# Optimization experiments

Hardware: AMD Instinct MI355X
Metric: run time of the kernel (lower is better)

## Reference

```python
import jax, jax.numpy as jnp
import numpy as np

N = 20000      # nodes
E = 640000     # edges
IN = 2         # in_dim
H = 4          # heads
C = 64         # hidden_dim (per-head channels)
ED = 3         # edge_dim
K = 4          # num_clusters
EPS = 1e-16    # PyG softmax eps


def setup_inputs():
    key = jax.random.key(0)
    ks = jax.random.split(key, 32)
    g = lambda i, sh: (jax.random.normal(ks[i], sh, dtype=jnp.float32) * 0.1)
    inp = {
        'x': jax.random.normal(ks[0], (N, IN), dtype=jnp.float32),
        'edge_index': jax.random.randint(ks[1], (2, E), 0, N, dtype=jnp.int64),
        'edge_attr': jax.random.normal(ks[2], (E, ED), dtype=jnp.float32),
        # input_proj
        'Wp': g(3, (IN, C)), 'bp': g(4, (C,)),
        # conv1: in C -> H*C, concat
        'W1': g(5, (C, H * C)), 'We1': g(6, (ED, H * C)),
        'as1': g(7, (H, C)), 'ad1': g(8, (H, C)), 'ae1': g(9, (H, C)), 'b1': g(10, (H * C,)),
        # conv2: in H*C -> H*C, concat
        'W2': g(11, (H * C, H * C)), 'We2': g(12, (ED, H * C)),
        'as2': g(13, (H, C)), 'ad2': g(14, (H, C)), 'ae2': g(15, (H, C)), 'b2': g(16, (H * C,)),
        # conv3: in H*C -> C, heads=1
        'W3': g(17, (H * C, C)), 'We3': g(18, (ED, C)),
        'as3': g(19, (1, C)), 'ad3': g(20, (1, C)), 'ae3': g(21, (1, C)), 'b3': g(22, (C,)),
        # classifier
        'Wc': g(23, (C, K)), 'bc': g(24, (K,)),
    }
    return inp


def _gat(h, src, dst, edge_attr, W, We, a_src, a_dst, a_edge, bias, heads, cph):
    """PyG GATConv (shared lin for src/dst, edge_dim, concat=True), eval mode."""
    xh = (h @ W).reshape(N, heads, cph)                       # [N,H,C]
    alpha_src = jnp.einsum('nhc,hc->nh', xh, a_src)           # [N,H]
    alpha_dst = jnp.einsum('nhc,hc->nh', xh, a_dst)
    eh = (edge_attr @ We).reshape(E, heads, cph)              # [E,H,C]
    alpha = alpha_src[src] + alpha_dst[dst] + jnp.einsum('ehc,hc->eh', eh, a_edge)
    alpha = jax.nn.leaky_relu(alpha, 0.2)                     # [E,H]
    # segment softmax over destination neighborhoods
    m = jax.ops.segment_max(alpha, dst, num_segments=N)       # [N,H]
    ea = jnp.exp(alpha - m[dst])
    s = jax.ops.segment_sum(ea, dst, num_segments=N)
    attn = ea / (s[dst] + EPS)                                # [E,H]
    msg = xh[src] * attn[:, :, None]                          # [E,H,C]
    out = jax.ops.segment_sum(msg, dst, num_segments=N)       # [N,H,C]
    return out.reshape(N, heads * cph) + bias


def reference(x, edge_index, edge_attr, Wp, bp,
              W1, We1, as1, ad1, ae1, b1,
              W2, We2, as2, ad2, ae2, b2,
              W3, We3, as3, ad3, ae3, b3,
              Wc, bc):
    src, dst = edge_index[0], edge_index[1]
    h = jax.nn.elu(x @ Wp + bp)
    h = jax.nn.elu(_gat(h, src, dst, edge_attr, W1, We1, as1, ad1, ae1, b1, H, C))
    h = jax.nn.elu(_gat(h, src, dst, edge_attr, W2, We2, as2, ad2, ae2, b2, H, C))
    h = _gat(h, src, dst, edge_attr, W3, We3, as3, ad3, ae3, b3, 1, C)
    return jax.nn.softmax(h @ Wc + bc, axis=-1)
```

## Files before the change

### kernel.cpp

```cpp
#include <hip/hip_runtime.h>
#include <math.h>

#define N_NODES 20000
#define N_EDGES 640000

typedef __attribute__((ext_vector_type(8))) short short8;
typedef __attribute__((ext_vector_type(4))) float floatx4;
typedef __attribute__((ext_vector_type(2))) float float2v;

__device__ __forceinline__ float elu_f(float v) { return v > 0.f ? v : expm1f(v); }

__device__ __forceinline__ unsigned short bf16_rne(float f) {
  union { float f; unsigned u; } v;
  v.f = f;
  unsigned r = v.u + 0x7FFF + ((v.u >> 16) & 1);
  return (unsigned short)(r >> 16);
}

__device__ __forceinline__ float bf_to_f(unsigned short u) {
  union { unsigned u; float f; } v;
  v.u = (unsigned)u << 16;
  return v.f;
}

__device__ __forceinline__ float2v unpack_bf2(unsigned u) {
  union { unsigned u; float f; } lo, hi;
  lo.u = u << 16;
  hi.u = u & 0xffff0000u;
  return (float2v){lo.f, hi.f};
}

__device__ __forceinline__ int swz(int c) {
  return (c & ~7) | ((((c & 7) + ((c >> 3) >> 2))) & 7);
}


__global__ void zero_int_kernel(int* p, int n) {
  int i = blockIdx.x * 256 + threadIdx.x;
  if (i < n) p[i] = 0;
}

__global__ void hist_kernel(const int* __restrict__ dst, int* __restrict__ cnt, int ne) {
  int e = blockIdx.x * 256 + threadIdx.x;
  if (e < ne) atomicAdd(&cnt[dst[e]], 1);
}

__global__ __launch_bounds__(1024) void scan_kernel(const int* __restrict__ cnt,
                                                    int* __restrict__ row_ptr,
                                                    int* __restrict__ row_next, int n) {
  __shared__ int part[1024];
  int t = threadIdx.x;
  int per = (n + 1023) / 1024;
  int base = t * per;
  int local = 0;
  for (int i = 0; i < per; ++i) {
    int idx = base + i;
    if (idx < n) local += cnt[idx];
  }
  part[t] = local;
  __syncthreads();
  for (int off = 1; off < 1024; off <<= 1) {
    int v = (t >= off) ? part[t - off] : 0;
    __syncthreads();
    part[t] += v;
    __syncthreads();
  }
  int prefix = (t == 0) ? 0 : part[t - 1];
  for (int i = 0; i < per; ++i) {
    int idx = base + i;
    if (idx < n) {
      row_ptr[idx] = prefix;
      row_next[idx] = prefix;
      prefix += cnt[idx];
    }
  }
  if (t == 1023) row_ptr[n] = part[1023];
}

__global__ void fill_kernel(const int* __restrict__ dst, int* __restrict__ row_next,
                            int* __restrict__ csr_eid, int ne) {
  int e = blockIdx.x * 256 + threadIdx.x;
  if (e >= ne) return;
  int pos = atomicAdd(&row_next[dst[e]], 1);
  csr_eid[pos] = e;
}


__global__ void prep_all_kernel(const float* __restrict__ x, const float* __restrict__ Wp,
                                const float* __restrict__ bp, unsigned short* __restrict__ h_bf,
                                const float* __restrict__ W1, const float* __restrict__ W2,
                                const float* __restrict__ W3, unsigned short* __restrict__ Bt1,
                                unsigned short* __restrict__ Bt2, unsigned short* __restrict__ Bt3,
                                const float* __restrict__ We1, const float* __restrict__ ae1,
                                const float* __restrict__ We2, const float* __restrict__ ae2,
                                const float* __restrict__ We3, const float* __restrict__ ae3,
                                float* __restrict__ proj) {
  int b = blockIdx.x, t = threadIdx.x;
  if (b < 5000) {
    int i = b * 256 + t;
    int node = i >> 6, c = i & 63;
    float v = x[node * 2] * Wp[c] + x[node * 2 + 1] * Wp[64 + c] + bp[c];
    h_bf[i] = bf16_rne(elu_f(v));
  } else if (b < 5384) {
    int idx = (b - 5000) * 256 + t;
    const float* W; unsigned short* Bt; int K, Nc, local;
    if (idx < 16384)      { W = W1; Bt = Bt1; K = 64;  Nc = 256; local = idx; }
    else if (idx < 81920) { W = W2; Bt = Bt2; K = 256; Nc = 256; local = idx - 16384; }
    else if (idx < 98304) { W = W3; Bt = Bt3; K = 256; Nc = 64;  local = idx - 81920; }
    else return;
    int k = local / Nc, n = local - k * Nc;
    Bt[(size_t)n * K + k] = bf16_rne(W[local]);
  } else {
    if (t < 12) {
      int d = t >> 2, h = t & 3;
      float s = 0.f;
      for (int c = 0; c < 64; ++c) s += We1[d * 256 + h * 64 + c] * ae1[h * 64 + c];
      proj[t] = s;
    } else if (t < 24) {
      int u = t - 12; int d = u >> 2, h = u & 3;
      float s = 0.f;
      for (int c = 0; c < 64; ++c) s += We2[d * 256 + h * 64 + c] * ae2[h * 64 + c];
      proj[12 + u] = s;
    } else if (t < 27) {
      int d = t - 24;
      float s = 0.f;
      for (int c = 0; c < 64; ++c) s += We3[d * 64 + c] * ae3[c];
      proj[24 + d] = s;
    }
  }
}


__global__ void edge_prep_kernel(const int* __restrict__ csr_eid, const int* __restrict__ src,
                                 const float* __restrict__ ea, const float* __restrict__ proj,
                                 int* __restrict__ csr_src, float* __restrict__ edot) {
  int i = blockIdx.x * 256 + threadIdx.x;
  if (i >= N_EDGES) return;
  int eid = csr_eid[i];
  csr_src[i] = src[eid];
  float e0 = ea[eid * 3 + 0], e1 = ea[eid * 3 + 1], e2 = ea[eid * 3 + 2];
  #pragma unroll
  for (int h = 0; h < 4; ++h)
    edot[(size_t)h * N_EDGES + i] = e0 * proj[h] + e1 * proj[4 + h] + e2 * proj[8 + h];
  #pragma unroll
  for (int h = 0; h < 4; ++h)
    edot[(size_t)(4 + h) * N_EDGES + i] = e0 * proj[12 + h] + e1 * proj[16 + h] + e2 * proj[20 + h];
  edot[(size_t)8 * N_EDGES + i] = e0 * proj[24] + e1 * proj[25] + e2 * proj[26];
}


template <int KDIM>
__global__ __launch_bounds__(256) void mfma_gemm_alpha_kernel(
    const unsigned short* __restrict__ A, const unsigned short* __restrict__ Bt,
    unsigned short* __restrict__ C_bf, const float* __restrict__ a_src,
    const float* __restrict__ a_dst, float* __restrict__ alp_s,
    float* __restrict__ alp_d, int M, int Nc) {
  __shared__ unsigned short As[64][40];
  __shared__ unsigned short Bs[64][40];
  int t = threadIdx.x;
  int wave = t >> 6, lane = t & 63;
  int m_frag = lane & 15, quad = lane >> 4;
  int row0 = blockIdx.y * 64, col0 = blockIdx.x * 64;
  int lr = t >> 2;
  int lk = (t & 3) * 8;
  floatx4 acc[4];
  #pragma unroll
  for (int c = 0; c < 4; ++c) acc[c] = (floatx4){0.f, 0.f, 0.f, 0.f};

  for (int k0 = 0; k0 < KDIM; k0 += 32) {
    int gr = row0 + lr;
    short8 av = {0, 0, 0, 0, 0, 0, 0, 0};
    if (gr < M) av = *(const short8*)(A + (size_t)gr * KDIM + k0 + lk);
    *(short8*)(&As[lr][lk]) = av;
    short8 bv = *(const short8*)(Bt + (size_t)(col0 + lr) * KDIM + k0 + lk);
    *(short8*)(&Bs[lr][lk]) = bv;
    __syncthreads();
    short8 a = *(const short8*)(&As[wave * 16 + m_frag][quad * 8]);
    #pragma unroll
    for (int c = 0; c < 4; ++c) {
      short8 b = *(const short8*)(&Bs[c * 16 + m_frag][quad * 8]);
      acc[c] = __builtin_amdgcn_mfma_f32_16x16x32_bf16(a, b, acc[c], 0, 0, 0);
    }
    __syncthreads();
  }

  int H = Nc >> 6;
  int head = blockIdx.x;
  float ps[4] = {}, pd[4] = {};
  #pragma unroll
  for (int c = 0; c < 4; ++c) {
    float asv = a_src[head * 64 + c * 16 + m_frag];
    float adv = a_dst[head * 64 + c * 16 + m_frag];
    #pragma unroll
    for (int i = 0; i < 4; ++i) {
      ps[i] += acc[c][i] * asv;
      pd[i] += acc[c][i] * adv;
    }
  }
  #pragma unroll
  for (int off = 1; off < 16; off <<= 1) {
    #pragma unroll
    for (int i = 0; i < 4; ++i) {
      ps[i] += __shfl_xor(ps[i], off);
      pd[i] += __shfl_xor(pd[i], off);
    }
  }
  #pragma unroll
  for (int c = 0; c < 4; ++c) {
    #pragma unroll
    for (int i = 0; i < 4; ++i) {
      int gr = row0 + wave * 16 + quad * 4 + i;
      if (gr < M) C_bf[(size_t)gr * Nc + col0 + c * 16 + m_frag] = bf16_rne(acc[c][i]);
    }
  }
  if (m_frag == 0) {
    #pragma unroll
    for (int i = 0; i < 4; ++i) {
      int gr = row0 + wave * 16 + quad * 4 + i;
      if (gr < M) {
        alp_s[gr * H + head] = ps[i];
        alp_d[gr * H + head] = pd[i];
      }
    }
  }
}


template <bool OUT_BF>
__global__ __launch_bounds__(256) void softagg4_kernel(
    const int* __restrict__ row_ptr, const int* __restrict__ csr_src,
    const float* __restrict__ edot, const float* __restrict__ alp_s,
    const float* __restrict__ alp_d, const unsigned short* __restrict__ xh_bf,
    const float* __restrict__ bias, float* __restrict__ out,
    unsigned short* __restrict__ out_bf) {
  constexpr int HC = 256, H = 4, CHUNK = 256, L = 32, S = 8;
  __shared__ float lds_w[H][CHUNK + 8];
  __shared__ int lds_src[CHUNK];
  __shared__ float sh_r[H];
  __shared__ float sh_inv[H];
  __shared__ float red[4 * HC];

  int n = blockIdx.x;
  int t = threadIdx.x;
  int wave = t >> 6, lane = t & 63;
  int slot = t / L, l = t % L;
  int head2 = (8 * l) >> 6;
  int s0 = row_ptr[n], s1 = row_ptr[n + 1];

  float m_run = -INFINITY, s_run = 0.f;
  float2v accp[4] = {};
  float adv = alp_d[n * H + wave];
  const float* __restrict__ edot_h = edot + (size_t)wave * N_EDGES;

  for (int c0 = s0; c0 < s1; c0 += CHUNK) {
    int cend = min(s1, c0 + CHUNK);
    {
      int h = wave;
      float cm = -INFINITY;
      for (int i = c0 + lane; i < cend; i += 64) {
        int s = csr_src[i];
        if (h == 0) lds_src[i - c0] = s;
        float a = alp_s[s * H + h] + adv + edot_h[i];
        a = a > 0.f ? a : 0.2f * a;
        lds_w[h][i - c0] = a;
        cm = fmaxf(cm, a);
      }
      #pragma unroll
      for (int off = 1; off < 64; off <<= 1) cm = fmaxf(cm, __shfl_xor(cm, off));
      float m_new = fmaxf(m_run, cm);
      float r = __expf(m_run - m_new);
      float se = 0.f;
      for (int i = c0 + lane; i < cend; i += 64) {
        float w = __expf(lds_w[h][i - c0] - m_new);
        lds_w[h][i - c0] = w;
        se += w;
      }
      #pragma unroll
      for (int off = 1; off < 64; off <<= 1) se += __shfl_xor(se, off);
      s_run = s_run * r + se;
      m_run = m_new;
      if (lane == 0) sh_r[h] = r;
    }
    __syncthreads();
    float2v rrp = {sh_r[head2], sh_r[head2]};
    #pragma unroll
    for (int d = 0; d < 4; ++d) accp[d] *= rrp;
    int i = c0 + slot;
    for (; i + S < cend; i += 2 * S) {
      int sA = lds_src[i - c0];
      int sB = lds_src[i - c0 + S];
      float wA = lds_w[head2][i - c0];
      float wB = lds_w[head2][i - c0 + S];
      uint4 uA = *(const uint4*)(xh_bf + (size_t)sA * HC + l * 8);
      uint4 uB = *(const uint4*)(xh_bf + (size_t)sB * HC + l * 8);
      float2v wAp = {wA, wA}, wBp = {wB, wB};
      accp[0] = __builtin_elementwise_fma(unpack_bf2(uA.x), wAp, accp[0]);
      accp[1] = __builtin_elementwise_fma(unpack_bf2(uA.y), wAp, accp[1]);
      accp[2] = __builtin_elementwise_fma(unpack_bf2(uA.z), wAp, accp[2]);
      accp[3] = __builtin_elementwise_fma(unpack_bf2(uA.w), wAp, accp[3]);
      accp[0] = __builtin_elementwise_fma(unpack_bf2(uB.x), wBp, accp[0]);
      accp[1] = __builtin_elementwise_fma(unpack_bf2(uB.y), wBp, accp[1]);
      accp[2] = __builtin_elementwise_fma(unpack_bf2(uB.z), wBp, accp[2]);
      accp[3] = __builtin_elementwise_fma(unpack_bf2(uB.w), wBp, accp[3]);
    }
    if (i < cend) {
      int s = lds_src[i - c0];
      float w = lds_w[head2][i - c0];
      uint4 u = *(const uint4*)(xh_bf + (size_t)s * HC + l * 8);
      float2v wp = {w, w};
      accp[0] = __builtin_elementwise_fma(unpack_bf2(u.x), wp, accp[0]);
      accp[1] = __builtin_elementwise_fma(unpack_bf2(u.y), wp, accp[1]);
      accp[2] = __builtin_elementwise_fma(unpack_bf2(u.z), wp, accp[2]);
      accp[3] = __builtin_elementwise_fma(unpack_bf2(u.w), wp, accp[3]);
    }
    __syncthreads();
  }
  if (lane == 0) sh_inv[wave] = 1.0f / (s_run + 1e-16f);
  __syncthreads();
  float2v invp = {sh_inv[head2], sh_inv[head2]};
  #pragma unroll
  for (int d = 0; d < 4; ++d) accp[d] *= invp;
  float accf[8];
  #pragma unroll
  for (int d = 0; d < 4; ++d) { accf[2 * d] = accp[d].x; accf[2 * d + 1] = accp[d].y; }
  #pragma unroll
  for (int off = L; off < 64; off <<= 1) {
    #pragma unroll
    for (int j = 0; j < 8; ++j) accf[j] += __shfl_xor(accf[j], off);
  }
  if (lane < L) {
    #pragma unroll
    for (int j = 0; j < 8; ++j) red[wave * HC + swz(lane * 8 + j)] = accf[j];
  }
  __syncthreads();
  {
    int pos = swz(t & (HC - 1));
    float a = red[0 * HC + pos] + red[1 * HC + pos] + red[2 * HC + pos] + red[3 * HC + pos];
    a += bias[t];
    a = elu_f(a);
    if (OUT_BF) out_bf[(size_t)n * HC + t] = bf16_rne(a);
    else out[(size_t)n * HC + t] = a;
  }
}


__global__ __launch_bounds__(256) void softagg_cls_kernel(
    const int* __restrict__ row_ptr, const int* __restrict__ csr_src,
    const float* __restrict__ edot, const float* __restrict__ alp_s,
    const float* __restrict__ alp_d, const unsigned short* __restrict__ xh_bf,
    const float* __restrict__ b3, const float* __restrict__ Wc,
    const float* __restrict__ bc, float* __restrict__ out, int n_nodes) {
  constexpr int CHUNK = 256;
  __shared__ float lds_w[4][CHUNK];
  __shared__ int lds_s[4][CHUNK];

  int wave = threadIdx.x >> 6, lane = threadIdx.x & 63;
  int n = blockIdx.x * 4 + wave;
  if (n >= n_nodes) return;
  int slot = lane >> 3, l = lane & 7;
  int s0 = row_ptr[n], s1 = row_ptr[n + 1];

  float m_run = -INFINITY, s_run = 0.f;
  float2v accp[4] = {};
  float adv = alp_d[n];

  for (int c0 = s0; c0 < s1; c0 += CHUNK) {
    int cend = min(s1, c0 + CHUNK);
    float cm = -INFINITY;
    for (int i = c0 + lane; i < cend; i += 64) {
      int s = csr_src[i];
      lds_s[wave][i - c0] = s;
      float a = alp_s[s] + adv + edot[i];
      a = a > 0.f ? a : 0.2f * a;
      lds_w[wave][i - c0] = a;
      cm = fmaxf(cm, a);
    }
    #pragma unroll
    for (int off = 1; off < 64; off <<= 1) cm = fmaxf(cm, __shfl_xor(cm, off));
    float m_new = fmaxf(m_run, cm);
    float r = __expf(m_run - m_new);
    float se = 0.f;
    for (int i = c0 + lane; i < cend; i += 64) {
      float w = __expf(lds_w[wave][i - c0] - m_new);
      lds_w[wave][i - c0] = w;
      se += w;
    }
    #pragma unroll
    for (int off = 1; off < 64; off <<= 1) se += __shfl_xor(se, off);
    s_run = s_run * r + se;
    m_run = m_new;
    float2v rp = {r, r};
    #pragma unroll
    for (int d = 0; d < 4; ++d) accp[d] *= rp;
    for (int i = c0 + slot; i < cend; i += 8) {
      int s = lds_s[wave][i - c0];
      float w = lds_w[wave][i - c0];
      uint4 u = *(const uint4*)(xh_bf + (size_t)s * 64 + l * 8);
      float2v wp = {w, w};
      accp[0] = __builtin_elementwise_fma(unpack_bf2(u.x), wp, accp[0]);
      accp[1] = __builtin_elementwise_fma(unpack_bf2(u.y), wp, accp[1]);
      accp[2] = __builtin_elementwise_fma(unpack_bf2(u.z), wp, accp[2]);
      accp[3] = __builtin_elementwise_fma(unpack_bf2(u.w), wp, accp[3]);
    }
  }
  float inv = 1.0f / (s_run + 1e-16f);
  float2v invp = {inv, inv};
  #pragma unroll
  for (int d = 0; d < 4; ++d) accp[d] *= invp;
  float accf[8];
  #pragma unroll
  for (int d = 0; d < 4; ++d) { accf[2 * d] = accp[d].x; accf[2 * d + 1] = accp[d].y; }
  #pragma unroll
  for (int off = 8; off < 64; off <<= 1) {
    #pragma unroll
    for (int j = 0; j < 8; ++j) accf[j] += __shfl_xor(accf[j], off);
  }
  float p0 = 0.f, p1 = 0.f, p2 = 0.f, p3 = 0.f;
  #pragma unroll
  for (int j = 0; j < 8; ++j) {
    int c = l * 8 + j;
    float v = accf[j] + b3[c];
    p0 += v * Wc[c * 4 + 0];
    p1 += v * Wc[c * 4 + 1];
    p2 += v * Wc[c * 4 + 2];
    p3 += v * Wc[c * 4 + 3];
  }
  #pragma unroll
  for (int off = 1; off < 8; off <<= 1) {
    p0 += __shfl_xor(p0, off);
    p1 += __shfl_xor(p1, off);
    p2 += __shfl_xor(p2, off);
    p3 += __shfl_xor(p3, off);
  }
  if (lane == 0) {
    p0 += bc[0]; p1 += bc[1]; p2 += bc[2]; p3 += bc[3];
    float mx = fmaxf(fmaxf(p0, p1), fmaxf(p2, p3));
    float e0 = __expf(p0 - mx), e1 = __expf(p1 - mx), e2 = __expf(p2 - mx), e3 = __expf(p3 - mx);
    float s = 1.f / (e0 + e1 + e2 + e3);
    out[n * 4 + 0] = e0 * s;
    out[n * 4 + 1] = e1 * s;
    out[n * 4 + 2] = e2 * s;
    out[n * 4 + 3] = e3 * s;
  }
}


extern "C" void kernel_launch(void* const* d_in, const int* in_sizes, int n_in,
                              void* d_out, int out_size, void* d_ws, size_t ws_size,
                              hipStream_t stream) {
  const float* x   = (const float*)d_in[0];
  const int*   ei  = (const int*)d_in[1];
  const float* ea  = (const float*)d_in[2];
  const float* Wp  = (const float*)d_in[3];
  const float* bp  = (const float*)d_in[4];
  const float* W1  = (const float*)d_in[5];
  const float* We1 = (const float*)d_in[6];
  const float* as1 = (const float*)d_in[7];
  const float* ad1 = (const float*)d_in[8];
  const float* ae1 = (const float*)d_in[9];
  const float* b1  = (const float*)d_in[10];
  const float* W2  = (const float*)d_in[11];
  const float* We2 = (const float*)d_in[12];
  const float* as2 = (const float*)d_in[13];
  const float* ad2 = (const float*)d_in[14];
  const float* ae2 = (const float*)d_in[15];
  const float* b2  = (const float*)d_in[16];
  const float* W3  = (const float*)d_in[17];
  const float* We3 = (const float*)d_in[18];
  const float* as3 = (const float*)d_in[19];
  const float* ad3 = (const float*)d_in[20];
  const float* ae3 = (const float*)d_in[21];
  const float* b3  = (const float*)d_in[22];
  const float* Wc  = (const float*)d_in[23];
  const float* bc  = (const float*)d_in[24];
  float* out = (float*)d_out;

  const int* src = ei;
  const int* dst = ei + N_EDGES;

  char* wptr = (char*)d_ws;
  auto alloc = [&](size_t bytes) {
    char* p = wptr;
    wptr += (bytes + 255) & ~(size_t)255;
    return p;
  };
  int*            cnt      = (int*)alloc((size_t)N_NODES * 4);
  int*            row_ptr  = (int*)alloc((size_t)(N_NODES + 1) * 4);
  int*            row_next = (int*)alloc((size_t)N_NODES * 4);
  int*            csr_eid  = (int*)alloc((size_t)N_EDGES * 4);
  int*            csr_src  = (int*)alloc((size_t)N_EDGES * 4);
  float*          edot     = (float*)alloc((size_t)9 * N_EDGES * 4);
  unsigned short* hA_bf    = (unsigned short*)alloc((size_t)N_NODES * 256 * 2);
  unsigned short* hX_bf    = (unsigned short*)alloc((size_t)N_NODES * 256 * 2);
  float*          alp_s    = (float*)alloc((size_t)N_NODES * 4 * 4);
  float*          alp_d    = (float*)alloc((size_t)N_NODES * 4 * 4);
  float*          proj     = (float*)alloc(32 * 4);
  unsigned short* Bt1      = (unsigned short*)alloc((size_t)64 * 256 * 2);
  unsigned short* Bt2      = (unsigned short*)alloc((size_t)256 * 256 * 2);
  unsigned short* Bt3      = (unsigned short*)alloc((size_t)256 * 64 * 2);

  zero_int_kernel<<<(N_NODES + 255) / 256, 256, 0, stream>>>(cnt, N_NODES);
  hist_kernel<<<(N_EDGES + 255) / 256, 256, 0, stream>>>(dst, cnt, N_EDGES);
  scan_kernel<<<1, 1024, 0, stream>>>(cnt, row_ptr, row_next, N_NODES);
  fill_kernel<<<(N_EDGES + 255) / 256, 256, 0, stream>>>(dst, row_next, csr_eid, N_EDGES);

  prep_all_kernel<<<5385, 256, 0, stream>>>(x, Wp, bp, hA_bf, W1, W2, W3, Bt1, Bt2, Bt3,
                                            We1, ae1, We2, ae2, We3, ae3, proj);
  edge_prep_kernel<<<(N_EDGES + 255) / 256, 256, 0, stream>>>(csr_eid, src, ea, proj,
                                                              csr_src, edot);

  dim3 g256(4, (N_NODES + 63) / 64);
  dim3 g64(1, (N_NODES + 63) / 64);

  mfma_gemm_alpha_kernel<64><<<g256, 256, 0, stream>>>(hA_bf, Bt1, hX_bf, as1, ad1,
                                                       alp_s, alp_d, N_NODES, 256);
  softagg4_kernel<true><<<N_NODES, 256, 0, stream>>>(row_ptr, csr_src,
                                                     edot + (size_t)0 * N_EDGES,
                                                     alp_s, alp_d, hX_bf, b1, nullptr, hA_bf);

  mfma_gemm_alpha_kernel<256><<<g256, 256, 0, stream>>>(hA_bf, Bt2, hX_bf, as2, ad2,
                                                        alp_s, alp_d, N_NODES, 256);
  softagg4_kernel<true><<<N_NODES, 256, 0, stream>>>(row_ptr, csr_src,
                                                     edot + (size_t)4 * N_EDGES,
                                                     alp_s, alp_d, hX_bf, b2, nullptr, hA_bf);

  mfma_gemm_alpha_kernel<256><<<g64, 256, 0, stream>>>(hA_bf, Bt3, hX_bf, as3, ad3,
                                                       alp_s, alp_d, N_NODES, 64);
  softagg_cls_kernel<<<(N_NODES + 3) / 4, 256, 0, stream>>>(row_ptr, csr_src,
                                                            edot + (size_t)8 * N_EDGES,
                                                            alp_s, alp_d, hX_bf, b3, Wc, bc,
                                                            out, N_NODES);
}
```

Measured before the change: 396.3 us.

## Fuse edge prep into prep kernel and widen per-lane gather in aggregation

Merges the edge-prep kernel into the prep kernel: each edge block recomputes the 27 edge projection scalars into shared memory rather than reading them from a separate global buffer, which removes one launch and a dependency. In the layer-1/2 aggregation kernel, each lane now gathers 16 bf16 channels (two 16-byte loads) with 16 edge slots instead of 8 channels with 8 slots. The final cross-wave reduction uses a padded 3D shared array in place of the swizzled buffer. The zeroing kernel is replaced by hipMemsetAsync. Recomputing the projections in every edge block adds redundant work, and the wider per-lane accumulators raise register pressure.

```diff
diff --git a/kernel.cpp b/kernel.cpp
--- a/kernel.cpp
+++ b/kernel.cpp
@@ -30,15 +30,6 @@
   return (float2v){lo.f, hi.f};
 }
 
-__device__ __forceinline__ int swz(int c) {
-  return (c & ~7) | ((((c & 7) + ((c >> 3) >> 2))) & 7);
-}
-
-
-__global__ void zero_int_kernel(int* p, int n) {
-  int i = blockIdx.x * 256 + threadIdx.x;
-  if (i < n) p[i] = 0;
-}
 
 __global__ void hist_kernel(const int* __restrict__ dst, int* __restrict__ cnt, int ne) {
   int e = blockIdx.x * 256 + threadIdx.x;
@@ -94,7 +85,9 @@
                                 const float* __restrict__ We1, const float* __restrict__ ae1,
                                 const float* __restrict__ We2, const float* __restrict__ ae2,
                                 const float* __restrict__ We3, const float* __restrict__ ae3,
-                                float* __restrict__ proj) {
+                                const int* __restrict__ csr_eid, const int* __restrict__ src,
+                                const float* __restrict__ ea, int* __restrict__ csr_src,
+                                float* __restrict__ edot) {
   int b = blockIdx.x, t = threadIdx.x;
   if (b < 5000) {
     int i = b * 256 + t;
@@ -111,41 +104,37 @@
     int k = local / Nc, n = local - k * Nc;
     Bt[(size_t)n * K + k] = bf16_rne(W[local]);
   } else {
+    __shared__ float pj[27];
     if (t < 12) {
       int d = t >> 2, h = t & 3;
       float s = 0.f;
       for (int c = 0; c < 64; ++c) s += We1[d * 256 + h * 64 + c] * ae1[h * 64 + c];
-      proj[t] = s;
+      pj[t] = s;
     } else if (t < 24) {
       int u = t - 12; int d = u >> 2, h = u & 3;
       float s = 0.f;
       for (int c = 0; c < 64; ++c) s += We2[d * 256 + h * 64 + c] * ae2[h * 64 + c];
-      proj[12 + u] = s;
+      pj[12 + u] = s;
     } else if (t < 27) {
       int d = t - 24;
       float s = 0.f;
       for (int c = 0; c < 64; ++c) s += We3[d * 64 + c] * ae3[c];
-      proj[24 + d] = s;
-    }
-  }
-}
-
-
-__global__ void edge_prep_kernel(const int* __restrict__ csr_eid, const int* __restrict__ src,
-                                 const float* __restrict__ ea, const float* __restrict__ proj,
-                                 int* __restrict__ csr_src, float* __restrict__ edot) {
-  int i = blockIdx.x * 256 + threadIdx.x;
-  if (i >= N_EDGES) return;
-  int eid = csr_eid[i];
-  csr_src[i] = src[eid];
-  float e0 = ea[eid * 3 + 0], e1 = ea[eid * 3 + 1], e2 = ea[eid * 3 + 2];
-  #pragma unroll
-  for (int h = 0; h < 4; ++h)
-    edot[(size_t)h * N_EDGES + i] = e0 * proj[h] + e1 * proj[4 + h] + e2 * proj[8 + h];
-  #pragma unroll
-  for (int h = 0; h < 4; ++h)
-    edot[(size_t)(4 + h) * N_EDGES + i] = e0 * proj[12 + h] + e1 * proj[16 + h] + e2 * proj[20 + h];
-  edot[(size_t)8 * N_EDGES + i] = e0 * proj[24] + e1 * proj[25] + e2 * proj[26];
+      pj[24 + d] = s;
+    }
+    __syncthreads();
+    int i = (b - 5384) * 256 + t;
+    if (i >= N_EDGES) return;
+    int eid = csr_eid[i];
+    csr_src[i] = src[eid];
+    float e0 = ea[eid * 3 + 0], e1 = ea[eid * 3 + 1], e2 = ea[eid * 3 + 2];
+    #pragma unroll
+    for (int h = 0; h < 4; ++h)
+      edot[(size_t)h * N_EDGES + i] = e0 * pj[h] + e1 * pj[4 + h] + e2 * pj[8 + h];
+    #pragma unroll
+    for (int h = 0; h < 4; ++h)
+      edot[(size_t)(4 + h) * N_EDGES + i] = e0 * pj[12 + h] + e1 * pj[16 + h] + e2 * pj[20 + h];
+    edot[(size_t)8 * N_EDGES + i] = e0 * pj[24] + e1 * pj[25] + e2 * pj[26];
+  }
 }
 
 
@@ -233,36 +222,35 @@
     const float* __restrict__ alp_d, const unsigned short* __restrict__ xh_bf,
     const float* __restrict__ bias, float* __restrict__ out,
     unsigned short* __restrict__ out_bf) {
-  constexpr int HC = 256, H = 4, CHUNK = 256, L = 32, S = 8;
+  constexpr int HC = 256, H = 4, CHUNK = 256, S = 16;
   __shared__ float lds_w[H][CHUNK + 8];
   __shared__ int lds_src[CHUNK];
   __shared__ float sh_r[H];
   __shared__ float sh_inv[H];
-  __shared__ float red[4 * HC];
+  __shared__ float red2[4][16][17];
 
   int n = blockIdx.x;
   int t = threadIdx.x;
   int wave = t >> 6, lane = t & 63;
-  int slot = t / L, l = t % L;
-  int head2 = (8 * l) >> 6;
+  int slot = t >> 4, l = t & 15;
+  int head2 = l >> 2;
   int s0 = row_ptr[n], s1 = row_ptr[n + 1];
 
   float m_run = -INFINITY, s_run = 0.f;
-  float2v accp[4] = {};
+  float2v accp[8] = {};
   float adv = alp_d[n * H + wave];
   const float* __restrict__ edot_h = edot + (size_t)wave * N_EDGES;
 
   for (int c0 = s0; c0 < s1; c0 += CHUNK) {
     int cend = min(s1, c0 + CHUNK);
     {
-      int h = wave;
       float cm = -INFINITY;
       for (int i = c0 + lane; i < cend; i += 64) {
         int s = csr_src[i];
-        if (h == 0) lds_src[i - c0] = s;
-        float a = alp_s[s * H + h] + adv + edot_h[i];
+        if (wave == 0) lds_src[i - c0] = s;
+        float a = alp_s[s * H + wave] + adv + edot_h[i];
         a = a > 0.f ? a : 0.2f * a;
-        lds_w[h][i - c0] = a;
+        lds_w[wave][i - c0] = a;
         cm = fmaxf(cm, a);
       }
       #pragma unroll
@@ -271,47 +259,65 @@
       float r = __expf(m_run - m_new);
       float se = 0.f;
       for (int i = c0 + lane; i < cend; i += 64) {
-        float w = __expf(lds_w[h][i - c0] - m_new);
-        lds_w[h][i - c0] = w;
+        float w = __expf(lds_w[wave][i - c0] - m_new);
+        lds_w[wave][i - c0] = w;
         se += w;
       }
       #pragma unroll
       for (int off = 1; off < 64; off <<= 1) se += __shfl_xor(se, off);
       s_run = s_run * r + se;
       m_run = m_new;
-      if (lane == 0) sh_r[h] = r;
+      if (lane == 0) sh_r[wave] = r;
     }
     __syncthreads();
     float2v rrp = {sh_r[head2], sh_r[head2]};
     #pragma unroll
-    for (int d = 0; d < 4; ++d) accp[d] *= rrp;
+    for (int d = 0; d < 8; ++d) accp[d] *= rrp;
     int i = c0 + slot;
     for (; i + S < cend; i += 2 * S) {
       int sA = lds_src[i - c0];
       int sB = lds_src[i - c0 + S];
       float wA = lds_w[head2][i - c0];
       float wB = lds_w[head2][i - c0 + S];
-      uint4 uA = *(const uint4*)(xh_bf + (size_t)sA * HC + l * 8);
-      uint4 uB = *(const uint4*)(xh_bf + (size_t)sB * HC + l * 8);
+      const uint4* pA = (const uint4*)(xh_bf + (size_t)sA * HC + l * 16);
+      const uint4* pB = (const uint4*)(xh_bf + (size_t)sB * HC + l * 16);
+      uint4 a0 = pA[0];
+      uint4 a1 = pA[1];
+      uint4 b0 = pB[0];
+      uint4 b1 = pB[1];
       float2v wAp = {wA, wA}, wBp = {wB, wB};
-      accp[0] = __builtin_elementwise_fma(unpack_bf2(uA.x), wAp, accp[0]);
-      accp[1] = __builtin_elementwise_fma(unpack_bf2(uA.y), wAp, accp[1]);
-      accp[2] = __builtin_elementwise_fma(unpack_bf2(uA.z), wAp, accp[2]);
-      accp[3] = __builtin_elementwise_fma(unpack_bf2(uA.w), wAp, accp[3]);
-      accp[0] = __builtin_elementwise_fma(unpack_bf2(uB.x), wBp, accp[0]);
-      accp[1] = __builtin_elementwise_fma(unpack_bf2(uB.y), wBp, accp[1]);
-      accp[2] = __builtin_elementwise_fma(unpack_bf2(uB.z), wBp, accp[2]);
-      accp[3] = __builtin_elementwise_fma(unpack_bf2(uB.w), wBp, accp[3]);
+      accp[0] = __builtin_elementwise_fma(unpack_bf2(a0.x), wAp, accp[0]);
+      accp[1] = __builtin_elementwise_fma(unpack_bf2(a0.y), wAp, accp[1]);
+      accp[2] = __builtin_elementwise_fma(unpack_bf2(a0.z), wAp, accp[2]);
+      accp[3] = __builtin_elementwise_fma(unpack_bf2(a0.w), wAp, accp[3]);
+      accp[4] = __builtin_elementwise_fma(unpack_bf2(a1.x), wAp, accp[4]);
+      accp[5] = __builtin_elementwise_fma(unpack_bf2(a1.y), wAp, accp[5]);
+      accp[6] = __builtin_elementwise_fma(unpack_bf2(a1.z), wAp, accp[6]);
+      accp[7] = __builtin_elementwise_fma(unpack_bf2(a1.w), wAp, accp[7]);
+      accp[0] = __builtin_elementwise_fma(unpack_bf2(b0.x), wBp, accp[0]);
+      accp[1] = __builtin_elementwise_fma(unpack_bf2(b0.y), wBp, accp[1]);
+      accp[2] = __builtin_elementwise_fma(unpack_bf2(b0.z), wBp, accp[2]);
+      accp[3] = __builtin_elementwise_fma(unpack_bf2(b0.w), wBp, accp[3]);
+      accp[4] = __builtin_elementwise_fma(unpack_bf2(b1.x), wBp, accp[4]);
+      accp[5] = __builtin_elementwise_fma(unpack_bf2(b1.y), wBp, accp[5]);
+      accp[6] = __builtin_elementwise_fma(unpack_bf2(b1.z), wBp, accp[6]);
+      accp[7] = __builtin_elementwise_fma(unpack_bf2(b1.w), wBp, accp[7]);
     }
     if (i < cend) {
       int s = lds_src[i - c0];
       float w = lds_w[head2][i - c0];
-      uint4 u = *(const uint4*)(xh_bf + (size_t)s * HC + l * 8);
+      const uint4* p = (const uint4*)(xh_bf + (size_t)s * HC + l * 16);
+      uint4 a0 = p[0];
+      uint4 a1 = p[1];
       float2v wp = {w, w};
-      accp[0] = __builtin_elementwise_fma(unpack_bf2(u.x), wp, accp[0]);
-      accp[1] = __builtin_elementwise_fma(unpack_bf2(u.y), wp, accp[1]);
-      accp[2] = __builtin_elementwise_fma(unpack_bf2(u.z), wp, accp[2]);
-      accp[3] = __builtin_elementwise_fma(unpack_bf2(u.w), wp, accp[3]);
+      accp[0] = __builtin_elementwise_fma(unpack_bf2(a0.x), wp, accp[0]);
+      accp[1] = __builtin_elementwise_fma(unpack_bf2(a0.y), wp, accp[1]);
+      accp[2] = __builtin_elementwise_fma(unpack_bf2(a0.z), wp, accp[2]);
+      accp[3] = __builtin_elementwise_fma(unpack_bf2(a0.w), wp, accp[3]);
+      accp[4] = __builtin_elementwise_fma(unpack_bf2(a1.x), wp, accp[4]);
+      accp[5] = __builtin_elementwise_fma(unpack_bf2(a1.y), wp, accp[5]);
+      accp[6] = __builtin_elementwise_fma(unpack_bf2(a1.z), wp, accp[6]);
+      accp[7] = __builtin_elementwise_fma(unpack_bf2(a1.w), wp, accp[7]);
     }
     __syncthreads();
   }
@@ -319,23 +325,23 @@
   __syncthreads();
   float2v invp = {sh_inv[head2], sh_inv[head2]};
   #pragma unroll
-  for (int d = 0; d < 4; ++d) accp[d] *= invp;
-  float accf[8];
-  #pragma unroll
-  for (int d = 0; d < 4; ++d) { accf[2 * d] = accp[d].x; accf[2 * d + 1] = accp[d].y; }
-  #pragma unroll
-  for (int off = L; off < 64; off <<= 1) {
-    #pragma unroll
-    for (int j = 0; j < 8; ++j) accf[j] += __shfl_xor(accf[j], off);
-  }
-  if (lane < L) {
-    #pragma unroll
-    for (int j = 0; j < 8; ++j) red[wave * HC + swz(lane * 8 + j)] = accf[j];
+  for (int d = 0; d < 8; ++d) accp[d] *= invp;
+  float accf[16];
+  #pragma unroll
+  for (int d = 0; d < 8; ++d) { accf[2 * d] = accp[d].x; accf[2 * d + 1] = accp[d].y; }
+  #pragma unroll
+  for (int off = 16; off < 64; off <<= 1) {
+    #pragma unroll
+    for (int j = 0; j < 16; ++j) accf[j] += __shfl_xor(accf[j], off);
+  }
+  if (lane < 16) {
+    #pragma unroll
+    for (int j = 0; j < 16; ++j) red2[wave][lane][j] = accf[j];
   }
   __syncthreads();
   {
-    int pos = swz(t & (HC - 1));
-    float a = red[0 * HC + pos] + red[1 * HC + pos] + red[2 * HC + pos] + red[3 * HC + pos];
+    int cl = t >> 4, cj = t & 15;
+    float a = red2[0][cl][cj] + red2[1][cl][cj] + red2[2][cl][cj] + red2[3][cl][cj];
     a += bias[t];
     a = elu_f(a);
     if (OUT_BF) out_bf[(size_t)n * HC + t] = bf16_rne(a);
@@ -494,20 +500,18 @@
   unsigned short* hX_bf    = (unsigned short*)alloc((size_t)N_NODES * 256 * 2);
   float*          alp_s    = (float*)alloc((size_t)N_NODES * 4 * 4);
   float*          alp_d    = (float*)alloc((size_t)N_NODES * 4 * 4);
-  float*          proj     = (float*)alloc(32 * 4);
   unsigned short* Bt1      = (unsigned short*)alloc((size_t)64 * 256 * 2);
   unsigned short* Bt2      = (unsigned short*)alloc((size_t)256 * 256 * 2);
   unsigned short* Bt3      = (unsigned short*)alloc((size_t)256 * 64 * 2);
 
-  zero_int_kernel<<<(N_NODES + 255) / 256, 256, 0, stream>>>(cnt, N_NODES);
+  hipMemsetAsync(cnt, 0, (size_t)N_NODES * 4, stream);
   hist_kernel<<<(N_EDGES + 255) / 256, 256, 0, stream>>>(dst, cnt, N_EDGES);
   scan_kernel<<<1, 1024, 0, stream>>>(cnt, row_ptr, row_next, N_NODES);
   fill_kernel<<<(N_EDGES + 255) / 256, 256, 0, stream>>>(dst, row_next, csr_eid, N_EDGES);
 
-  prep_all_kernel<<<5385, 256, 0, stream>>>(x, Wp, bp, hA_bf, W1, W2, W3, Bt1, Bt2, Bt3,
-                                            We1, ae1, We2, ae2, We3, ae3, proj);
-  edge_prep_kernel<<<(N_EDGES + 255) / 256, 256, 0, stream>>>(csr_eid, src, ea, proj,
-                                                              csr_src, edot);
+  prep_all_kernel<<<5384 + (N_EDGES + 255) / 256, 256, 0, stream>>>(
+      x, Wp, bp, hA_bf, W1, W2, W3, Bt1, Bt2, Bt3,
+      We1, ae1, We2, ae2, We3, ae3, csr_eid, src, ea, csr_src, edot);
 
   dim3 g256(4, (N_NODES + 63) / 64);
   dim3 g64(1, (N_NODES + 63) / 64);
```

Result: slower. 450.4 us (+13.6%).
